# Optimization experiments

Measured on AMD Instinct MI355X. Metric: run time of the kernel, lower is better.

The kernel has to match this reference:

```python
import jax, jax.numpy as jnp
import numpy as np
import math

B, N, DIM = 4, 2048, 768
HEADS, DIM_HEAD = 12, 64
SCALE = math.sqrt(DIM_HEAD)


def setup_inputs() -> dict:
    key = jax.random.key(0)
    ks = jax.random.split(key, 5)
    inner = HEADS * DIM_HEAD
    x = jax.random.normal(ks[0], (B, N, DIM), dtype=jnp.float32)
    # Linear weights stored as [in, out] so y = x @ W (equivalent to torch Linear with W.T)
    w_q = jax.random.normal(ks[1], (DIM, inner), dtype=jnp.float32) * 0.02
    w_k = jax.random.normal(ks[2], (DIM, inner), dtype=jnp.float32) * 0.02
    w_v = jax.random.normal(ks[3], (DIM, inner), dtype=jnp.float32) * 0.02
    w_o = jax.random.normal(ks[4], (inner, DIM), dtype=jnp.float32) * 0.02
    b_o = jnp.zeros((DIM,), dtype=jnp.float32)
    return {"x": x, "w_q": w_q, "w_k": w_k, "w_v": w_v, "w_o": w_o, "b_o": b_o}


def _split_heads(t):
    # [b, n, h*d] -> [b, h, n, d]
    b, n, _ = t.shape
    return t.reshape(b, n, HEADS, DIM_HEAD).transpose(0, 2, 1, 3)


def reference(x, w_q, w_k, w_v, w_o, b_o):
    # context = x (self-attention, kv_include_self=False)
    q = _split_heads(x @ w_q)  # [b,h,n,d]
    k = _split_heads(x @ w_k)
    v = _split_heads(x @ w_v)
    scores = jnp.einsum("bhnd,bhmd->bhnm", q, k) / SCALE  # [b,h,n,n]
    attn = jax.nn.softmax(scores, axis=-1)  # dropout p=0 -> identity
    h = jnp.einsum("bhnm,bhmd->bhnd", attn, v)  # [b,h,n,d]
    H = h.transpose(0, 2, 1, 3).reshape(x.shape[0], x.shape[1], HEADS * DIM_HEAD)
    out = H @ w_o + b_o
    return out
```

## Files before the change

### kernel.cpp

```cpp
#include <hip/hip_runtime.h>
#include <hip/hip_bf16.h>
#include <cstdint>
#include <cstddef>

#define HEADS 12
#define DHEAD 64
#define SEQ   2048
#define DIMM  768
#define BATCH 4
#define MROWS (BATCH*SEQ)
#define BH    (BATCH*HEADS)
#define QT    (SEQ/128)
#define SCL_Q 0.18033688011112042f
#define M2FIX 6.0f

typedef __attribute__((ext_vector_type(8))) short short8;
typedef __attribute__((ext_vector_type(4))) short short4v;
typedef __attribute__((ext_vector_type(4))) float floatx4;

__device__ __forceinline__ unsigned short f2bf(float f) {
    union { float f; uint32_t u; } v; v.f = f;
    uint32_t u = v.u;
    u += 0x7fffu + ((u >> 16) & 1u);
    return (unsigned short)(u >> 16);
}
__device__ __forceinline__ float bf2f(unsigned short h) {
    union { uint32_t u; float f; } v; v.u = ((uint32_t)h) << 16;
    return v.f;
}
__device__ __forceinline__ uint32_t pkbf(float a, float b) {
    __hip_bfloat162 h = __float22bfloat162_rn(make_float2(a, b));
    uint32_t u; __builtin_memcpy(&u, &h, 4); return u;
}
__device__ __forceinline__ float fexp2(float x) {
#if __has_builtin(__builtin_amdgcn_exp2f)
    return __builtin_amdgcn_exp2f(x);
#else
    return exp2f(x);
#endif
}

#if __has_builtin(__builtin_amdgcn_global_load_lds)
#define HAVE_GLDS 1
__device__ __forceinline__ void glds16(const unsigned short* g, unsigned short* l) {
    __builtin_amdgcn_global_load_lds(
        (const __attribute__((address_space(1))) unsigned int*)g,
        (__attribute__((address_space(3))) unsigned int*)l, 16, 0, 0);
}
#else
#define HAVE_GLDS 0
#endif

__global__ void detect_dtype(const uint32_t* __restrict__ xw, int* __restrict__ flag) {
    __shared__ int cnt;
    if (threadIdx.x == 0) cnt = 0;
    __syncthreads();
    uint32_t w = xw[(size_t)threadIdx.x * 4096];
    float v = bf2f((unsigned short)(w & 0xFFFFu));
    float av = fabsf(v);
    int ok = (av >= 9.0949e-13f && av <= 256.0f) ? 1 : 0;
    atomicAdd(&cnt, ok);
    __syncthreads();
    if (threadIdx.x == 0) *flag = (cnt >= 192) ? 0 : 1;
}

__global__ __launch_bounds__(256) void convert_x(
    const void* __restrict__ xin, unsigned short* __restrict__ xc,
    const int* __restrict__ flag)
{
    const int isf32 = *flag;
    const size_t i0 = ((size_t)blockIdx.x * 256 + threadIdx.x) * 8;
    if (isf32) {
        const float* xf = (const float*)xin;
        float4 a = *(const float4*)&xf[i0];
        float4 b = *(const float4*)&xf[i0 + 4];
        short8 s = { (short)f2bf(a.x), (short)f2bf(a.y), (short)f2bf(a.z), (short)f2bf(a.w),
                     (short)f2bf(b.x), (short)f2bf(b.y), (short)f2bf(b.z), (short)f2bf(b.w) };
        *(short8*)&xc[i0] = s;
    } else {
        *(short8*)&xc[i0] = *(const short8*)&((const unsigned short*)xin)[i0];
    }
}

__global__ __launch_bounds__(256) void transpose_w(
    const void* __restrict__ wq, const void* __restrict__ wk,
    const void* __restrict__ wv, const void* __restrict__ wo,
    unsigned short* __restrict__ wtq, unsigned short* __restrict__ wtk,
    unsigned short* __restrict__ wtv, unsigned short* __restrict__ wto,
    const int* __restrict__ flag)
{
    __shared__ unsigned short tile[32][33];
    const int isf32 = *flag;
    const void* src;
    unsigned short* dst;
    switch (blockIdx.z) {
        case 0: src = wq; dst = wtq; break;
        case 1: src = wk; dst = wtk; break;
        case 2: src = wv; dst = wtv; break;
        default: src = wo; dst = wto; break;
    }
    const float* srcf = (const float*)src;
    const unsigned short* srcs = (const unsigned short*)src;
    const int tx = threadIdx.x;
    const int ty = threadIdx.y;
    const int k0 = blockIdx.x * 32;
    const int n0 = blockIdx.y * 32;
    #pragma unroll
    for (int it = 0; it < 4; it++) {
        int r = ty + it * 8;
        size_t idx = (size_t)(k0 + r) * DIMM + n0 + tx;
        tile[r][tx] = isf32 ? f2bf(srcf[idx]) : srcs[idx];
    }
    __syncthreads();
    #pragma unroll
    for (int it = 0; it < 4; it++) {
        int r = ty + it * 8;
        dst[(size_t)(n0 + r) * DIMM + k0 + tx] = tile[tx][r];
    }
}

__global__ __launch_bounds__(256) void gemm_bt(
    const unsigned short* __restrict__ A,
    const unsigned short* __restrict__ Wt0,
    const unsigned short* __restrict__ Wt1,
    const unsigned short* __restrict__ Wt2,
    void* __restrict__ O0, void* __restrict__ O1, void* __restrict__ O2,
    const void* __restrict__ bias,
    const int* __restrict__ flag,
    int mode_base)
{
    const int mode = mode_base + blockIdx.z;
    const unsigned short* Wt = (mode == 1) ? Wt1 : (mode == 2) ? Wt2 : Wt0;
    void* OutV               = (mode == 1) ? O1  : (mode == 2) ? O2  : O0;
    unsigned short* Out16 = (unsigned short*)OutV;
    float* Outf           = (float*)OutV;
    const int isf32 = *flag;

    __shared__ unsigned short As[128 * 64];
    __shared__ unsigned short Bs[128 * 64];

    const int tid  = threadIdx.x;
    const int wid  = tid >> 6;
    const int lane = tid & 63;
    const int l16  = lane & 15;
    const int quad = lane >> 4;
    const int wm   = wid & 1;
    const int wn   = wid >> 1;
    const int bm   = blockIdx.x * 128;
    const int bn   = blockIdx.y * 128;

    floatx4 acc[4][4];
    #pragma unroll
    for (int i = 0; i < 4; i++)
        #pragma unroll
        for (int j = 0; j < 4; j++)
            acc[i][j] = floatx4{0.f, 0.f, 0.f, 0.f};

    for (int kk = 0; kk < DIMM; kk += 64) {
        #pragma unroll
        for (int t = 0; t < 4; t++) {
            const int c  = t * 256 + tid;
            const int r  = c >> 3;
            const int lc = (((c & 7) ^ (r & 7))) * 8;
#if HAVE_GLDS
            glds16(&A [(size_t)(bm + r) * DIMM + kk + lc], &As[(t * 256 + wid * 64) * 8]);
            glds16(&Wt[(size_t)(bn + r) * DIMM + kk + lc], &Bs[(t * 256 + wid * 64) * 8]);
#else
            *(short8*)&As[c * 8] = *(const short8*)&A [(size_t)(bm + r) * DIMM + kk + lc];
            *(short8*)&Bs[c * 8] = *(const short8*)&Wt[(size_t)(bn + r) * DIMM + kk + lc];
#endif
        }
        __syncthreads();
        #pragma unroll
        for (int ks = 0; ks < 2; ks++) {
            const int ph = ((ks * 4 + quad) ^ (l16 & 7)) * 8;
            short8 af[4], bf[4];
            #pragma unroll
            for (int t = 0; t < 4; t++)
                af[t] = *(const short8*)&As[(wm * 64 + t * 16 + l16) * 64 + ph];
            #pragma unroll
            for (int t = 0; t < 4; t++)
                bf[t] = *(const short8*)&Bs[(wn * 64 + t * 16 + l16) * 64 + ph];
            #pragma unroll
            for (int mt = 0; mt < 4; mt++)
                #pragma unroll
                for (int nt = 0; nt < 4; nt++)
                    acc[mt][nt] = __builtin_amdgcn_mfma_f32_16x16x32_bf16(
                        af[mt], bf[nt], acc[mt][nt], 0, 0, 0);
        }
        __syncthreads();
    }

    #pragma unroll
    for (int nt = 0; nt < 4; nt++) {
        const int gcol = bn + wn * 64 + nt * 16 + l16;
        float bv = 0.f;
        if (mode == 3)
            bv = isf32 ? ((const float*)bias)[gcol]
                       : bf2f(((const unsigned short*)bias)[gcol]);
        #pragma unroll
        for (int mt = 0; mt < 4; mt++) {
            if (mode == 2) {
                const int grow0 = bm + wm * 64 + mt * 16 + quad * 4;
                const int b = grow0 >> 11, n0 = grow0 & 2047;
                const int h = gcol >> 6,  d  = gcol & 63;
                size_t addr = ((size_t)(b * HEADS + h) * DHEAD + d) * SEQ + n0;
                short4v pk = { (short)f2bf(acc[mt][nt][0]), (short)f2bf(acc[mt][nt][1]),
                               (short)f2bf(acc[mt][nt][2]), (short)f2bf(acc[mt][nt][3]) };
                *(short4v*)&Out16[addr] = pk;
            } else {
                #pragma unroll
                for (int i = 0; i < 4; i++) {
                    const int grow = bm + wm * 64 + mt * 16 + quad * 4 + i;
                    float v = acc[mt][nt][i];
                    if (mode == 0) v *= SCL_Q;
                    if (mode == 3) v += bv;
                    if (mode == 3) {
                        size_t addr = (size_t)grow * DIMM + gcol;
                        if (isf32) Outf[addr] = v;
                        else       Out16[addr] = f2bf(v);
                    } else {
                        const int b = grow >> 11, n = grow & 2047;
                        const int h = gcol >> 6,  d = gcol & 63;
                        Out16[((size_t)(b * HEADS + h) * SEQ + n) * DHEAD + d] = f2bf(v);
                    }
                }
            }
        }
    }
}

__global__ __launch_bounds__(256) void attn(
    const unsigned short* __restrict__ Q,
    const unsigned short* __restrict__ K,
    const unsigned short* __restrict__ Vt,
    unsigned short* __restrict__ Hout)
{
    __shared__ unsigned short Ks[64 * 72];
    __shared__ unsigned short Vs[64 * 72];
    __shared__ unsigned short Ps[8 * 16 * 72];

    const int tid  = threadIdx.x;
    const int wid  = tid >> 6;
    const int lane = tid & 63;
    const int l16  = lane & 15;
    const int quad = lane >> 4;

    const int bh = blockIdx.x % BH;
    const int qt = blockIdx.x / BH;

    short8 qf[2][2];
    #pragma unroll
    for (int t = 0; t < 2; t++) {
        const int qrow = qt * 128 + wid * 32 + t * 16 + l16;
        const size_t qbase = ((size_t)bh * SEQ + qrow) * DHEAD;
        qf[t][0] = *(const short8*)&Q[qbase + quad * 8];
        qf[t][1] = *(const short8*)&Q[qbase + 32 + quad * 8];
    }

    float l_acc[2] = {0.f, 0.f};
    floatx4 ot[2][4];
    #pragma unroll
    for (int t = 0; t < 2; t++)
        #pragma unroll
        for (int i = 0; i < 4; i++) ot[t][i] = floatx4{0.f, 0.f, 0.f, 0.f};

    const size_t kbase = (size_t)bh * SEQ * DHEAD;
    const size_t vbase = (size_t)bh * DHEAD * SEQ;
    unsigned short* Pw0 = &Ps[(wid * 2 + 0) * 16 * 72];
    unsigned short* Pw1 = &Ps[(wid * 2 + 1) * 16 * 72];

    short8 rk[2], rv[2];
    {
        #pragma unroll
        for (int j = 0; j < 2; j++) {
            const int c = tid + j * 256, r = c >> 3, c8 = (c & 7) * 8;
            rk[j] = *(const short8*)&K[kbase + (size_t)r * DHEAD + c8];
            rv[j] = *(const short8*)&Vt[vbase + (size_t)r * SEQ + c8];
        }
    }

    for (int kt = 0; kt < SEQ / 64; kt++) {
        __syncthreads();
        #pragma unroll
        for (int j = 0; j < 2; j++) {
            const int c = tid + j * 256, r = c >> 3, c8 = (c & 7) * 8;
            *(short8*)&Ks[r * 72 + c8] = rk[j];
            *(short8*)&Vs[r * 72 + c8] = rv[j];
        }
        __syncthreads();
        if (kt + 1 < SEQ / 64) {
            #pragma unroll
            for (int j = 0; j < 2; j++) {
                const int c = tid + j * 256, r = c >> 3, c8 = (c & 7) * 8;
                rk[j] = *(const short8*)&K[kbase + (size_t)((kt + 1) * 64 + r) * DHEAD + c8];
                rv[j] = *(const short8*)&Vt[vbase + (size_t)r * SEQ + (kt + 1) * 64 + c8];
            }
        }

        floatx4 st[2][4];
        #pragma unroll
        for (int mt = 0; mt < 4; mt++) {
            short8 kf0 = *(const short8*)&Ks[(mt * 16 + l16) * 72 + quad * 8];
            short8 kf1 = *(const short8*)&Ks[(mt * 16 + l16) * 72 + 32 + quad * 8];
            #pragma unroll
            for (int t = 0; t < 2; t++) {
                floatx4 a = floatx4{0.f, 0.f, 0.f, 0.f};
                a = __builtin_amdgcn_mfma_f32_16x16x32_bf16(kf0, qf[t][0], a, 0, 0, 0);
                a = __builtin_amdgcn_mfma_f32_16x16x32_bf16(kf1, qf[t][1], a, 0, 0, 0);
                st[t][mt] = a;
            }
        }

        #pragma unroll
        for (int t = 0; t < 2; t++) {
            unsigned short* Pw = t ? Pw1 : Pw0;
            #pragma unroll
            for (int mt = 0; mt < 4; mt++) {
                float p0 = fexp2(st[t][mt][0] - M2FIX);
                float p1 = fexp2(st[t][mt][1] - M2FIX);
                float p2 = fexp2(st[t][mt][2] - M2FIX);
                float p3 = fexp2(st[t][mt][3] - M2FIX);
                l_acc[t] += (p0 + p1) + (p2 + p3);
                uint2 pk = { pkbf(p0, p1), pkbf(p2, p3) };
                *(uint2*)&Pw[l16 * 72 + mt * 16 + quad * 4] = pk;
            }
        }

        #pragma unroll
        for (int ks = 0; ks < 2; ks++) {
            short8 pf0 = *(const short8*)&Pw0[l16 * 72 + ks * 32 + quad * 8];
            short8 pf1 = *(const short8*)&Pw1[l16 * 72 + ks * 32 + quad * 8];
            #pragma unroll
            for (int dt = 0; dt < 4; dt++) {
                short8 vf = *(const short8*)&Vs[(dt * 16 + l16) * 72 + ks * 32 + quad * 8];
                ot[0][dt] = __builtin_amdgcn_mfma_f32_16x16x32_bf16(vf, pf0, ot[0][dt], 0, 0, 0);
                ot[1][dt] = __builtin_amdgcn_mfma_f32_16x16x32_bf16(vf, pf1, ot[1][dt], 0, 0, 0);
            }
        }
    }

    const int b = bh / HEADS, h = bh % HEADS;
    #pragma unroll
    for (int t = 0; t < 2; t++) {
        float l = l_acc[t];
        l += __shfl_xor(l, 16);
        l += __shfl_xor(l, 32);
        const float inv_l = 1.0f / l;
        unsigned short* Pw = t ? Pw1 : Pw0;
        #pragma unroll
        for (int dt = 0; dt < 4; dt++) {
            uint2 pk = { pkbf(ot[t][dt][0] * inv_l, ot[t][dt][1] * inv_l),
                         pkbf(ot[t][dt][2] * inv_l, ot[t][dt][3] * inv_l) };
            *(uint2*)&Pw[l16 * 72 + dt * 16 + quad * 4] = pk;
        }
        const int q_r   = lane >> 2;
        const int dpart = (lane & 3) * 16;
        short8 h0 = *(const short8*)&Pw[q_r * 72 + dpart];
        short8 h1 = *(const short8*)&Pw[q_r * 72 + dpart + 8];
        const int growg = b * SEQ + qt * 128 + wid * 32 + t * 16 + q_r;
        const size_t oaddr = (size_t)growg * DIMM + h * DHEAD + dpart;
        *(short8*)&Hout[oaddr] = h0;
        *(short8*)&Hout[oaddr + 8] = h1;
    }
}

extern "C" void kernel_launch(void* const* d_in, const int* in_sizes, int n_in,
                              void* d_out, int out_size, void* d_ws, size_t ws_size,
                              hipStream_t stream)
{
    (void)in_sizes; (void)n_in; (void)out_size;
    const void* x  = d_in[0];
    const void* wq = d_in[1];
    const void* wk = d_in[2];
    const void* wv = d_in[3];
    const void* wo = d_in[4];
    const void* bo = d_in[5];

    char* ws = (char*)d_ws;
    const size_t SZ_QKV = (size_t)MROWS * DIMM * sizeof(unsigned short);
    const size_t SZ_W   = (size_t)DIMM * DIMM * sizeof(unsigned short);
    const size_t need = 256 + 5 * SZ_QKV + 4 * SZ_W;
    if (ws_size < need) return;

    int* flag = (int*)ws;
    unsigned short* xc   = (unsigned short*)(ws + 256);
    unsigned short* Qws  = (unsigned short*)(ws + 256 + SZ_QKV);
    unsigned short* Kws  = (unsigned short*)(ws + 256 + 2 * SZ_QKV);
    unsigned short* Vtws = (unsigned short*)(ws + 256 + 3 * SZ_QKV);
    unsigned short* Hws  = (unsigned short*)(ws + 256 + 4 * SZ_QKV);
    unsigned short* Wtq  = (unsigned short*)(ws + 256 + 5 * SZ_QKV);
    unsigned short* Wtk  = (unsigned short*)(ws + 256 + 5 * SZ_QKV + SZ_W);
    unsigned short* Wtv  = (unsigned short*)(ws + 256 + 5 * SZ_QKV + 2 * SZ_W);
    unsigned short* Wto  = (unsigned short*)(ws + 256 + 5 * SZ_QKV + 3 * SZ_W);

    hipLaunchKernelGGL(detect_dtype, dim3(1), dim3(256), 0, stream,
                       (const uint32_t*)x, flag);
    hipLaunchKernelGGL(convert_x, dim3(MROWS * DIMM / 2048), dim3(256), 0, stream,
                       x, xc, flag);
    hipLaunchKernelGGL(transpose_w, dim3(24, 24, 4), dim3(32, 8), 0, stream,
                       wq, wk, wv, wo, Wtq, Wtk, Wtv, Wto, flag);
    hipLaunchKernelGGL(gemm_bt, dim3(64, 6, 3), dim3(256), 0, stream,
                       xc, Wtq, Wtk, Wtv, (void*)Qws, (void*)Kws, (void*)Vtws,
                       bo, flag, 0);
    hipLaunchKernelGGL(attn, dim3(BH * QT), dim3(256), 0, stream,
                       Qws, Kws, Vtws, Hws);
    hipLaunchKernelGGL(gemm_bt, dim3(64, 6, 1), dim3(256), 0, stream,
                       Hws, Wto, Wto, Wto, d_out, d_out, d_out, bo, flag, 3);
}
```

Before: 252.0 us.

## Fuse prep kernels, recompute dtype flag per block, swap MFMA operands for vector stores

Merges dtype detection, x conversion and weight transposition into one prep kernel, with every block re-running the dtype detection instead of reading a flag written by a separate launch. In the Q/K and output GEMMs the MFMA operands are swapped so each lane holds four consecutive output columns, which allows vectorized 4-wide stores and vectorized bias loads in place of scalar stores. This is meant to cut launch count and epilogue store traffic. In exchange every prep block and every output-GEMM block spends extra sampled global reads and an LDS atomic on detection.

```diff
diff --git a/kernel.cpp b/kernel.cpp
--- a/kernel.cpp
+++ b/kernel.cpp
@@ -51,71 +51,68 @@
 #define HAVE_GLDS 0
 #endif
 
-__global__ void detect_dtype(const uint32_t* __restrict__ xw, int* __restrict__ flag) {
-    __shared__ int cnt;
-    if (threadIdx.x == 0) cnt = 0;
+__device__ __forceinline__ int detect_f32(const uint32_t* xw, int tid) {
+    __shared__ int cnt_;
+    if (tid == 0) cnt_ = 0;
     __syncthreads();
-    uint32_t w = xw[(size_t)threadIdx.x * 4096];
-    float v = bf2f((unsigned short)(w & 0xFFFFu));
-    float av = fabsf(v);
-    int ok = (av >= 9.0949e-13f && av <= 256.0f) ? 1 : 0;
-    atomicAdd(&cnt, ok);
+    uint32_t w = xw[(size_t)(tid & 255) * 4096];
+    float av = fabsf(bf2f((unsigned short)(w & 0xFFFFu)));
+    atomicAdd(&cnt_, (av >= 9.0949e-13f && av <= 256.0f) ? 1 : 0);
     __syncthreads();
-    if (threadIdx.x == 0) *flag = (cnt >= 192) ? 0 : 1;
-}
-
-__global__ __launch_bounds__(256) void convert_x(
-    const void* __restrict__ xin, unsigned short* __restrict__ xc,
-    const int* __restrict__ flag)
-{
-    const int isf32 = *flag;
-    const size_t i0 = ((size_t)blockIdx.x * 256 + threadIdx.x) * 8;
-    if (isf32) {
-        const float* xf = (const float*)xin;
-        float4 a = *(const float4*)&xf[i0];
-        float4 b = *(const float4*)&xf[i0 + 4];
-        short8 s = { (short)f2bf(a.x), (short)f2bf(a.y), (short)f2bf(a.z), (short)f2bf(a.w),
-                     (short)f2bf(b.x), (short)f2bf(b.y), (short)f2bf(b.z), (short)f2bf(b.w) };
-        *(short8*)&xc[i0] = s;
-    } else {
-        *(short8*)&xc[i0] = *(const short8*)&((const unsigned short*)xin)[i0];
-    }
-}
-
-__global__ __launch_bounds__(256) void transpose_w(
+    return (cnt_ < 192) ? 1 : 0;
+}
+
+__global__ __launch_bounds__(256) void prep(
+    const void* __restrict__ x,
     const void* __restrict__ wq, const void* __restrict__ wk,
     const void* __restrict__ wv, const void* __restrict__ wo,
+    unsigned short* __restrict__ xc,
     unsigned short* __restrict__ wtq, unsigned short* __restrict__ wtk,
-    unsigned short* __restrict__ wtv, unsigned short* __restrict__ wto,
-    const int* __restrict__ flag)
+    unsigned short* __restrict__ wtv, unsigned short* __restrict__ wto)
 {
-    __shared__ unsigned short tile[32][33];
-    const int isf32 = *flag;
-    const void* src;
-    unsigned short* dst;
-    switch (blockIdx.z) {
-        case 0: src = wq; dst = wtq; break;
-        case 1: src = wk; dst = wtk; break;
-        case 2: src = wv; dst = wtv; break;
-        default: src = wo; dst = wto; break;
-    }
-    const float* srcf = (const float*)src;
-    const unsigned short* srcs = (const unsigned short*)src;
-    const int tx = threadIdx.x;
-    const int ty = threadIdx.y;
-    const int k0 = blockIdx.x * 32;
-    const int n0 = blockIdx.y * 32;
-    #pragma unroll
-    for (int it = 0; it < 4; it++) {
-        int r = ty + it * 8;
-        size_t idx = (size_t)(k0 + r) * DIMM + n0 + tx;
-        tile[r][tx] = isf32 ? f2bf(srcf[idx]) : srcs[idx];
-    }
-    __syncthreads();
-    #pragma unroll
-    for (int it = 0; it < 4; it++) {
-        int r = ty + it * 8;
-        dst[(size_t)(n0 + r) * DIMM + k0 + tx] = tile[tx][r];
+    const int tid = threadIdx.x;
+    const int isf32 = detect_f32((const uint32_t*)x, tid);
+    const int blk = blockIdx.x;
+
+    if (blk < 2304) {
+        __shared__ unsigned short tile[32][33];
+        const int m = blk / 576, rr = blk % 576;
+        const void* src; unsigned short* dst;
+        switch (m) {
+            case 0: src = wq; dst = wtq; break;
+            case 1: src = wk; dst = wtk; break;
+            case 2: src = wv; dst = wtv; break;
+            default: src = wo; dst = wto; break;
+        }
+        const float* srcf = (const float*)src;
+        const unsigned short* srcs = (const unsigned short*)src;
+        const int tx = tid & 31, ty = tid >> 5;
+        const int k0 = (rr % 24) * 32;
+        const int n0 = (rr / 24) * 32;
+        #pragma unroll
+        for (int it = 0; it < 4; it++) {
+            int r = ty + it * 8;
+            size_t idx = (size_t)(k0 + r) * DIMM + n0 + tx;
+            tile[r][tx] = isf32 ? f2bf(srcf[idx]) : srcs[idx];
+        }
+        __syncthreads();
+        #pragma unroll
+        for (int it = 0; it < 4; it++) {
+            int r = ty + it * 8;
+            dst[(size_t)(n0 + r) * DIMM + k0 + tx] = tile[tx][r];
+        }
+    } else {
+        const size_t i0 = ((size_t)(blk - 2304) * 256 + tid) * 8;
+        if (isf32) {
+            const float* xf = (const float*)x;
+            float4 a = *(const float4*)&xf[i0];
+            float4 b = *(const float4*)&xf[i0 + 4];
+            short8 s = { (short)f2bf(a.x), (short)f2bf(a.y), (short)f2bf(a.z), (short)f2bf(a.w),
+                         (short)f2bf(b.x), (short)f2bf(b.y), (short)f2bf(b.z), (short)f2bf(b.w) };
+            *(short8*)&xc[i0] = s;
+        } else {
+            *(short8*)&xc[i0] = *(const short8*)&((const unsigned short*)x)[i0];
+        }
     }
 }
 
@@ -126,7 +123,7 @@
     const unsigned short* __restrict__ Wt2,
     void* __restrict__ O0, void* __restrict__ O1, void* __restrict__ O2,
     const void* __restrict__ bias,
-    const int* __restrict__ flag,
+    const uint32_t* __restrict__ xsample,
     int mode_base)
 {
     const int mode = mode_base + blockIdx.z;
@@ -134,7 +131,9 @@
     void* OutV               = (mode == 1) ? O1  : (mode == 2) ? O2  : O0;
     unsigned short* Out16 = (unsigned short*)OutV;
     float* Outf           = (float*)OutV;
-    const int isf32 = *flag;
+
+    int isf32 = 0;
+    if (mode == 3) isf32 = detect_f32(xsample, threadIdx.x);
 
     __shared__ unsigned short As[128 * 64];
     __shared__ unsigned short Bs[128 * 64];
@@ -148,6 +147,7 @@
     const int wn   = wid >> 1;
     const int bm   = blockIdx.x * 128;
     const int bn   = blockIdx.y * 128;
+    const bool swap = (mode != 2);
 
     floatx4 acc[4][4];
     #pragma unroll
@@ -174,33 +174,38 @@
         #pragma unroll
         for (int ks = 0; ks < 2; ks++) {
             const int ph = ((ks * 4 + quad) ^ (l16 & 7)) * 8;
-            short8 af[4], bf[4];
+            short8 xa[4], wb[4];
             #pragma unroll
             for (int t = 0; t < 4; t++)
-                af[t] = *(const short8*)&As[(wm * 64 + t * 16 + l16) * 64 + ph];
+                xa[t] = *(const short8*)&As[(wm * 64 + t * 16 + l16) * 64 + ph];
             #pragma unroll
             for (int t = 0; t < 4; t++)
-                bf[t] = *(const short8*)&Bs[(wn * 64 + t * 16 + l16) * 64 + ph];
-            #pragma unroll
-            for (int mt = 0; mt < 4; mt++)
+                wb[t] = *(const short8*)&Bs[(wn * 64 + t * 16 + l16) * 64 + ph];
+            if (swap) {
                 #pragma unroll
-                for (int nt = 0; nt < 4; nt++)
-                    acc[mt][nt] = __builtin_amdgcn_mfma_f32_16x16x32_bf16(
-                        af[mt], bf[nt], acc[mt][nt], 0, 0, 0);
+                for (int mt = 0; mt < 4; mt++)
+                    #pragma unroll
+                    for (int nt = 0; nt < 4; nt++)
+                        acc[mt][nt] = __builtin_amdgcn_mfma_f32_16x16x32_bf16(
+                            wb[mt], xa[nt], acc[mt][nt], 0, 0, 0);
+            } else {
+                #pragma unroll
+                for (int mt = 0; mt < 4; mt++)
+                    #pragma unroll
+                    for (int nt = 0; nt < 4; nt++)
+                        acc[mt][nt] = __builtin_amdgcn_mfma_f32_16x16x32_bf16(
+                            xa[mt], wb[nt], acc[mt][nt], 0, 0, 0);
+            }
         }
         __syncthreads();
     }
 
-    #pragma unroll
-    for (int nt = 0; nt < 4; nt++) {
-        const int gcol = bn + wn * 64 + nt * 16 + l16;
-        float bv = 0.f;
-        if (mode == 3)
-            bv = isf32 ? ((const float*)bias)[gcol]
-                       : bf2f(((const unsigned short*)bias)[gcol]);
-        #pragma unroll
-        for (int mt = 0; mt < 4; mt++) {
-            if (mode == 2) {
+    if (!swap) {
+        #pragma unroll
+        for (int nt = 0; nt < 4; nt++) {
+            const int gcol = bn + wn * 64 + nt * 16 + l16;
+            #pragma unroll
+            for (int mt = 0; mt < 4; mt++) {
                 const int grow0 = bm + wm * 64 + mt * 16 + quad * 4;
                 const int b = grow0 >> 11, n0 = grow0 & 2047;
                 const int h = gcol >> 6,  d  = gcol & 63;
@@ -208,22 +213,38 @@
                 short4v pk = { (short)f2bf(acc[mt][nt][0]), (short)f2bf(acc[mt][nt][1]),
                                (short)f2bf(acc[mt][nt][2]), (short)f2bf(acc[mt][nt][3]) };
                 *(short4v*)&Out16[addr] = pk;
-            } else {
-                #pragma unroll
-                for (int i = 0; i < 4; i++) {
-                    const int grow = bm + wm * 64 + mt * 16 + quad * 4 + i;
-                    float v = acc[mt][nt][i];
-                    if (mode == 0) v *= SCL_Q;
-                    if (mode == 3) v += bv;
-                    if (mode == 3) {
-                        size_t addr = (size_t)grow * DIMM + gcol;
-                        if (isf32) Outf[addr] = v;
-                        else       Out16[addr] = f2bf(v);
+            }
+        }
+    } else {
+        #pragma unroll
+        for (int nt = 0; nt < 4; nt++) {
+            const int grow = bm + wm * 64 + nt * 16 + l16;
+            #pragma unroll
+            for (int mt = 0; mt < 4; mt++) {
+                const int gcol0 = bn + wn * 64 + mt * 16 + quad * 4;
+                float v0 = acc[mt][nt][0], v1 = acc[mt][nt][1];
+                float v2 = acc[mt][nt][2], v3 = acc[mt][nt][3];
+                if (mode == 0) { v0 *= SCL_Q; v1 *= SCL_Q; v2 *= SCL_Q; v3 *= SCL_Q; }
+                if (mode == 3) {
+                    if (isf32) {
+                        float4 bv = *(const float4*)&((const float*)bias)[gcol0];
+                        float4 o = { v0 + bv.x, v1 + bv.y, v2 + bv.z, v3 + bv.w };
+                        *(float4*)&Outf[(size_t)grow * DIMM + gcol0] = o;
                     } else {
-                        const int b = grow >> 11, n = grow & 2047;
-                        const int h = gcol >> 6,  d = gcol & 63;
-                        Out16[((size_t)(b * HEADS + h) * SEQ + n) * DHEAD + d] = f2bf(v);
+                        const unsigned short* bb = &((const unsigned short*)bias)[gcol0];
+                        short4v pk = { (short)f2bf(v0 + bf2f(bb[0])),
+                                       (short)f2bf(v1 + bf2f(bb[1])),
+                                       (short)f2bf(v2 + bf2f(bb[2])),
+                                       (short)f2bf(v3 + bf2f(bb[3])) };
+                        *(short4v*)&Out16[(size_t)grow * DIMM + gcol0] = pk;
                     }
+                } else {
+                    const int b = grow >> 11, n = grow & 2047;
+                    const int h = gcol0 >> 6, d = gcol0 & 63;
+                    size_t addr = ((size_t)(b * HEADS + h) * SEQ + n) * DHEAD + d;
+                    short4v pk = { (short)f2bf(v0), (short)f2bf(v1),
+                                   (short)f2bf(v2), (short)f2bf(v3) };
+                    *(short4v*)&Out16[addr] = pk;
                 }
             }
         }
@@ -271,13 +292,11 @@
     unsigned short* Pw1 = &Ps[(wid * 2 + 1) * 16 * 72];
 
     short8 rk[2], rv[2];
-    {
-        #pragma unroll
-        for (int j = 0; j < 2; j++) {
-            const int c = tid + j * 256, r = c >> 3, c8 = (c & 7) * 8;
-            rk[j] = *(const short8*)&K[kbase + (size_t)r * DHEAD + c8];
-            rv[j] = *(const short8*)&Vt[vbase + (size_t)r * SEQ + c8];
-        }
+    #pragma unroll
+    for (int j = 0; j < 2; j++) {
+        const int c = tid + j * 256, r = c >> 3, c8 = (c & 7) * 8;
+        rk[j] = *(const short8*)&K[kbase + (size_t)r * DHEAD + c8];
+        rv[j] = *(const short8*)&Vt[vbase + (size_t)r * SEQ + c8];
     }
 
     for (int kt = 0; kt < SEQ / 64; kt++) {
@@ -380,31 +399,27 @@
     char* ws = (char*)d_ws;
     const size_t SZ_QKV = (size_t)MROWS * DIMM * sizeof(unsigned short);
     const size_t SZ_W   = (size_t)DIMM * DIMM * sizeof(unsigned short);
-    const size_t need = 256 + 5 * SZ_QKV + 4 * SZ_W;
+    const size_t need = 5 * SZ_QKV + 4 * SZ_W;
     if (ws_size < need) return;
 
-    int* flag = (int*)ws;
-    unsigned short* xc   = (unsigned short*)(ws + 256);
-    unsigned short* Qws  = (unsigned short*)(ws + 256 + SZ_QKV);
-    unsigned short* Kws  = (unsigned short*)(ws + 256 + 2 * SZ_QKV);
-    unsigned short* Vtws = (unsigned short*)(ws + 256 + 3 * SZ_QKV);
-    unsigned short* Hws  = (unsigned short*)(ws + 256 + 4 * SZ_QKV);
-    unsigned short* Wtq  = (unsigned short*)(ws + 256 + 5 * SZ_QKV);
-    unsigned short* Wtk  = (unsigned short*)(ws + 256 + 5 * SZ_QKV + SZ_W);
-    unsigned short* Wtv  = (unsigned short*)(ws + 256 + 5 * SZ_QKV + 2 * SZ_W);
-    unsigned short* Wto  = (unsigned short*)(ws + 256 + 5 * SZ_QKV + 3 * SZ_W);
-
-    hipLaunchKernelGGL(detect_dtype, dim3(1), dim3(256), 0, stream,
-                       (const uint32_t*)x, flag);
-    hipLaunchKernelGGL(convert_x, dim3(MROWS * DIMM / 2048), dim3(256), 0, stream,
-                       x, xc, flag);
-    hipLaunchKernelGGL(transpose_w, dim3(24, 24, 4), dim3(32, 8), 0, stream,
-                       wq, wk, wv, wo, Wtq, Wtk, Wtv, Wto, flag);
+    unsigned short* xc   = (unsigned short*)(ws);
+    unsigned short* Qws  = (unsigned short*)(ws + 1 * SZ_QKV);
+    unsigned short* Kws  = (unsigned short*)(ws + 2 * SZ_QKV);
+    unsigned short* Vtws = (unsigned short*)(ws + 3 * SZ_QKV);
+    unsigned short* Hws  = (unsigned short*)(ws + 4 * SZ_QKV);
+    unsigned short* Wtq  = (unsigned short*)(ws + 5 * SZ_QKV);
+    unsigned short* Wtk  = (unsigned short*)(ws + 5 * SZ_QKV + SZ_W);
+    unsigned short* Wtv  = (unsigned short*)(ws + 5 * SZ_QKV + 2 * SZ_W);
+    unsigned short* Wto  = (unsigned short*)(ws + 5 * SZ_QKV + 3 * SZ_W);
+
+    hipLaunchKernelGGL(prep, dim3(2304 + MROWS * DIMM / 2048), dim3(256), 0, stream,
+                       x, wq, wk, wv, wo, xc, Wtq, Wtk, Wtv, Wto);
     hipLaunchKernelGGL(gemm_bt, dim3(64, 6, 3), dim3(256), 0, stream,
                        xc, Wtq, Wtk, Wtv, (void*)Qws, (void*)Kws, (void*)Vtws,
-                       bo, flag, 0);
+                       bo, (const uint32_t*)x, 0);
     hipLaunchKernelGGL(attn, dim3(BH * QT), dim3(256), 0, stream,
                        Qws, Kws, Vtws, Hws);
     hipLaunchKernelGGL(gemm_bt, dim3(64, 6, 1), dim3(256), 0, stream,
-                       Hws, Wto, Wto, Wto, d_out, d_out, d_out, bo, flag, 3);
-}
+                       Hws, Wto, Wto, Wto, d_out, d_out, d_out,
+                       bo, (const uint32_t*)x, 3);
+}
```

Result: no change. 248.1 us (-1.5%).
